# Kernel tuning notes

Measured on AMD Instinct MI355X. Metric: run time of the kernel, lower is better.

Reference implementation:

```python
import jax, jax.numpy as jnp
import numpy as np

B, D, FH, FW, C = 8, 41, 32, 88, 64
OGFH, OGFW = 512, 1408
DX = jnp.array([0.5, 20.0, 0.5], dtype=jnp.float32)          # voxel sizes (x, y, z)
BX = jnp.array([-49.75, 0.0, -49.75], dtype=jnp.float32)    # voxel centers origin
NX = (200, 1, 200)                                           # grid dims (x, y, z)
NSEG = NX[0] * NX[1] * NX[2] * B                             # 320000 voxel-batch slots


def _frustum():
    # (D, FH, FW, 3) pixel-u, pixel-v, depth; matches create_frustum_1camera
    ds = jnp.broadcast_to(jnp.arange(4.0, 45.0, 1.0)[:, None, None], (D, FH, FW))
    xs = jnp.broadcast_to(jnp.linspace(0.0, OGFW - 1, FW)[None, None, :], (D, FH, FW))
    ys = jnp.broadcast_to(jnp.linspace(0.0, OGFH - 1, FH)[None, :, None], (D, FH, FW))
    return jnp.stack([xs, ys, ds], axis=-1).astype(jnp.float32)


def setup_inputs() -> dict:
    key = jax.random.key(0)
    k1, = jax.random.split(key, 1)
    x = jax.random.normal(k1, (B, D, FH, FW, C), dtype=jnp.float32)
    # realistic pinhole intrinsics: fx=fy=800, principal point at image center
    K = np.array([[800.0, 0.0, OGFW / 2.0],
                  [0.0, 800.0, OGFH / 2.0],
                  [0.0, 0.0, 1.0]], dtype=np.float32)
    intrins = jnp.asarray(np.broadcast_to(K, (B, 3, 3)).copy())
    post_rots = jnp.broadcast_to(jnp.eye(3, dtype=jnp.float32), (B, 3, 3)) + jnp.zeros((B, 3, 3), jnp.float32)
    post_trans = jnp.zeros((B, 3), dtype=jnp.float32)
    return {"x": x, "intrins": intrins, "post_rots": post_rots, "post_trans": post_trans}


def _forward(x, intrins, post_rots, post_trans):
    # ---- get_geometry ----
    pts = _frustum()[None] - post_trans[:, None, None, None, :]          # (B,D,FH,FW,3)
    pts = jnp.einsum('bij,bdhwj->bdhwi', jnp.linalg.inv(post_rots), pts)
    pts = jnp.concatenate([pts[..., :2] * pts[..., 2:3], pts[..., 2:3]], axis=-1)
    geom = jnp.einsum('bij,bdhwj->bdhwi', jnp.linalg.inv(intrins), pts)  # camera-frame xyz

    # ---- voxel_splat ----
    Nprime = B * D * FH * FW
    xf = x.reshape(Nprime, C)
    # torch .long() truncates toward zero -> float->int cast in jnp also truncates
    coords = ((geom - (BX - DX / 2.0)) / DX).reshape(Nprime, 3).astype(jnp.int32)
    batch_ix = jnp.repeat(jnp.arange(B, dtype=jnp.int32), Nprime // B)
    kept = ((coords[:, 0] >= 0) & (coords[:, 0] < NX[0]) &
            (coords[:, 1] >= 0) & (coords[:, 1] < NX[1]) &
            (coords[:, 2] >= 0) & (coords[:, 2] < NX[2]))
    ranks = (coords[:, 0] * (NX[1] * NX[2] * B) + coords[:, 1] * (NX[2] * B) +
             coords[:, 2] * B + batch_ix)
    ranks = jnp.where(kept, ranks, NSEG)  # dump out-of-grid points into extra segment
    # segment-sum == sort + cumsum-trick pooling (sum of features per voxel)
    pooled = jax.ops.segment_sum(xf, ranks, num_segments=NSEG + 1)[:-1]  # (NSEG, C)
    final = pooled.reshape(NX[0], NX[1], NX[2], B, C)       # rank order: (x, y, z, b)
    final = jnp.transpose(final, (3, 4, 1, 2, 0))            # (B, C, ny, nz, nx)
    # torch.cat(final.unbind(dim=2), 1) -> stack ny slices along channel dim
    out = jnp.transpose(final, (0, 2, 1, 3, 4)).reshape(B, NX[1] * C, NX[2], NX[0])
    return out


def reference(x, intrins, post_rots, post_trans):
    return _forward(x, intrins, post_rots, post_trans)
```

## Files before the change

### kernel.cpp

```cpp
#include <hip/hip_runtime.h>

#define BB 8
#define DD 41
#define FHH 32
#define FWW 88
#define CC 64
#define NXX 200
#define NXZ 200
#define PLANE (NXZ * NXX)
#define WG 8
#define NWG (FWW / WG)
#define NBD (BB * DD)
#define NTILE (NBD * NWG)
#define NROWS (BB * NXZ)
#define PAD 204
#define STEPX (1407.0f / 87.0f)
#define STEPY (511.0f / 31.0f)

#define TSN    (NBD * FWW * CC)
#define MM_OFF TSN
#define CX_OFF (MM_OFF + NBD * FWW)
#define RD_OFF (CX_OFF + NBD * FWW)

__device__ __forceinline__ void inv3x3(const float* __restrict__ a, float* o) {
#pragma clang fp contract(off)
    float c00 = a[4] * a[8] - a[5] * a[7];
    float c01 = a[5] * a[6] - a[3] * a[8];
    float c02 = a[3] * a[7] - a[4] * a[6];
    float det = a[0] * c00 + a[1] * c01 + a[2] * c02;
    o[0] = c00 / det;
    o[1] = (a[2] * a[7] - a[1] * a[8]) / det;
    o[2] = (a[1] * a[5] - a[2] * a[4]) / det;
    o[3] = c01 / det;
    o[4] = (a[0] * a[8] - a[2] * a[6]) / det;
    o[5] = (a[2] * a[3] - a[0] * a[5]) / det;
    o[6] = c02 / det;
    o[7] = (a[1] * a[6] - a[0] * a[7]) / det;
    o[8] = (a[0] * a[4] - a[1] * a[3]) / det;
}

__device__ __forceinline__ int cz_of(const float* iR, const float* iK,
                                     float t0, float t1, float t2, int d) {
#pragma clang fp contract(off)
    float dv = 4.0f + (float)d;
    float q0 = 0.0f - t0, q1 = 0.0f - t1, q2 = dv - t2;
    float p0 = fmaf(iR[2], q2, fmaf(iR[1], q1, iR[0] * q0));
    float p1 = fmaf(iR[5], q2, fmaf(iR[4], q1, iR[3] * q0));
    float p2 = fmaf(iR[8], q2, fmaf(iR[7], q1, iR[6] * q0));
    float s0 = p0 * p2, s1 = p1 * p2, s2 = p2;
    float g2 = fmaf(iK[8], s2, fmaf(iK[7], s1, iK[6] * s0));
    float czf = (g2 + 50.0f) * 2.0f;
    return (int)czf;
}

__global__ __launch_bounds__(256) void lss_meta(
        const float* __restrict__ intrins, const float* __restrict__ post_rots,
        const float* __restrict__ post_trans, int* __restrict__ wsI) {
#pragma clang fp contract(off)
    __shared__ float sInv[18];
    int bd = blockIdx.x;
    int d = bd % DD, b = bd / DD;
    int tid = threadIdx.x;
    if (tid == 0) {
        inv3x3(post_rots + b * 9, sInv);
        inv3x3(intrins  + b * 9, sInv + 9);
    }
    __syncthreads();
    const float* iR = sInv;
    const float* iK = sInv + 9;
    float t0 = post_trans[b * 3 + 0];
    float t1 = post_trans[b * 3 + 1];
    float t2 = post_trans[b * 3 + 2];
    float dv = 4.0f + (float)d;
    unsigned* maskW = (unsigned*)wsI + MM_OFF;
    int* cxW  = wsI + CX_OFF;
    int* rowD = wsI + RD_OFF;

    for (int t = tid; t < FWW * FHH; t += 256) {
        int w = t >> 5;
        int h = t & 31;
        float u = (float)w * STEPX;
        float v = (float)h * STEPY;
        float q0 = u - t0, q1 = v - t1, q2 = dv - t2;
        float p0 = fmaf(iR[2], q2, fmaf(iR[1], q1, iR[0] * q0));
        float p1 = fmaf(iR[5], q2, fmaf(iR[4], q1, iR[3] * q0));
        float p2 = fmaf(iR[8], q2, fmaf(iR[7], q1, iR[6] * q0));
        float s0 = p0 * p2, s1 = p1 * p2, s2 = p2;
        float g0 = fmaf(iK[2], s2, fmaf(iK[1], s1, iK[0] * s0));
        float g1 = fmaf(iK[5], s2, fmaf(iK[4], s1, iK[3] * s0));
        float g2 = fmaf(iK[8], s2, fmaf(iK[7], s1, iK[6] * s0));
        float cxf = (g0 + 50.0f) * 2.0f;
        float cyf = (g1 + 10.0f) / 20.0f;
        float czf = (g2 + 50.0f) * 2.0f;
        int cx = (int)cxf;
        int cy = (int)cyf;
        int cz = (int)czf;
        bool kept = (cx >= 0) & (cx < NXX) & (cy == 0) & (cz >= 0) & (cz < NXZ);
        unsigned long long m = __ballot(kept);
        int lane = tid & 63;
        int cxc = min(NXX - 1, max(0, cx));
        if (lane == 0) {
            maskW[bd * FWW + w] = (unsigned)m;
            cxW[bd * FWW + w]   = cxc;
        } else if (lane == 32) {
            maskW[bd * FWW + w] = (unsigned)(m >> 32);
            cxW[bd * FWW + w]   = cxc;
        }
    }
    if (tid == 0) {
        int cz = cz_of(iR, iK, t0, t1, t2, d);
        if (cz >= 0 && cz < NXZ) rowD[b * NXZ + cz] = d;
    }
}

__global__ __launch_bounds__(512) void lss_tiles(
        const float* __restrict__ x, const int* __restrict__ wsI,
        float* __restrict__ wsF) {
#pragma clang fp contract(off)
    int blk = blockIdx.x;
    int tid = threadIdx.x;
    int wg = blk % NWG;
    int bd = blk / NWG;
    int wv   = tid >> 6;
    int lane = tid & 63;
    int cq   = lane & 15;
    int hsub = lane >> 4;
    int w = wg * WG + wv;

    unsigned m = ((const unsigned*)wsI)[MM_OFF + bd * FWW + w];
    const float* colp = x + ((size_t)bd * FHH * FWW + w) * CC + cq * 4;

    float4 vals[8];
#pragma unroll
    for (int hh = 0; hh < 8; ++hh)
        vals[hh] = *reinterpret_cast<const float4*>(
            colp + (size_t)(hh * 4 + hsub) * (FWW * CC));

    float4 acc = make_float4(0.f, 0.f, 0.f, 0.f);
#pragma unroll
    for (int hh = 0; hh < 8; ++hh) {
        bool bt = (m >> (hh * 4 + hsub)) & 1u;
        acc.x += bt ? vals[hh].x : 0.0f;
        acc.y += bt ? vals[hh].y : 0.0f;
        acc.z += bt ? vals[hh].z : 0.0f;
        acc.w += bt ? vals[hh].w : 0.0f;
    }
#pragma unroll
    for (int mm = 16; mm <= 32; mm <<= 1) {
        acc.x += __shfl_xor(acc.x, mm, 64);
        acc.y += __shfl_xor(acc.y, mm, 64);
        acc.z += __shfl_xor(acc.z, mm, 64);
        acc.w += __shfl_xor(acc.w, mm, 64);
    }
    if (hsub == 0)
        *reinterpret_cast<float4*>(wsF + ((size_t)(bd * FWW + w)) * CC + cq * 4) = acc;
}

__global__ __launch_bounds__(256) void lss_rows(
        const int* __restrict__ wsI, const float* __restrict__ wsF,
        float* __restrict__ out) {
#pragma clang fp contract(off)
    __shared__ float srow[CC * PAD];
    __shared__ int scx[FWW];
    int blk = blockIdx.x;
    int b = blk / NXZ, czr = blk % NXZ;
    int tid = threadIdx.x;
    int d = wsI[RD_OFF + blk];
    size_t outBase = ((size_t)b * CC) * PLANE + (size_t)czr * NXX;

    if (d < 0 || d >= DD) {
        float4 z = make_float4(0.f, 0.f, 0.f, 0.f);
        for (int i = tid; i < CC * (NXX / 4); i += 256) {
            int c = i / (NXX / 4), q = i - c * (NXX / 4);
            *reinterpret_cast<float4*>(out + outBase + (size_t)c * PLANE + q * 4) = z;
        }
        return;
    }
    int bd = b * DD + d;
    for (int i = tid; i < CC * PAD; i += 256) srow[i] = 0.0f;
    if (tid < FWW) scx[tid] = wsI[CX_OFF + bd * FWW + tid];
    __syncthreads();

    for (int i = tid; i < FWW * CC; i += 256) {
        int w = i >> 6, ch = i & 63;
        float v = wsF[(size_t)(bd * FWW + w) * CC + ch];
        atomicAdd(&srow[ch * PAD + scx[w]], v);
    }
    __syncthreads();

    for (int i = tid; i < CC * (NXX / 4); i += 256) {
        int c = i / (NXX / 4), q = i - c * (NXX / 4);
        *reinterpret_cast<float4*>(out + outBase + (size_t)c * PLANE + q * 4) =
            *reinterpret_cast<const float4*>(&srow[c * PAD + q * 4]);
    }
}

extern "C" void kernel_launch(void* const* d_in, const int* in_sizes, int n_in,
                              void* d_out, int out_size, void* d_ws, size_t ws_size,
                              hipStream_t stream) {
    const float* x          = (const float*)d_in[0];
    const float* intrins    = (const float*)d_in[1];
    const float* post_rots  = (const float*)d_in[2];
    const float* post_trans = (const float*)d_in[3];
    float* out = (float*)d_out;
    int*   wsI = (int*)d_ws;
    float* wsF = (float*)d_ws;

    lss_meta <<<NBD,   256, 0, stream>>>(intrins, post_rots, post_trans, wsI);
    lss_tiles<<<NTILE, 512, 0, stream>>>(x, wsI, wsF);
    lss_rows <<<NROWS, 256, 0, stream>>>(wsI, wsF, out);
}
```

Baseline: 88.41 us.

## Fuse column reduction and row scatter into one kernel split by cx halves

Merges the tile-reduction and row-writing kernels into one launch. Each (b,d) slice is handled by two blocks that cover the lower and upper cx range around a midpoint computed in the meta kernel. Each block reduces its columns and accumulates them with shared-memory atomics, then writes the output row directly. Extra blocks zero the rows that no depth covers, and they recompute that coverage themselves. This removes the intermediate workspace round-trip and one launch, but each slice now runs on at most two blocks, which lowers parallelism, and the output writes become scalar.

```diff
diff --git a/kernel.cpp b/kernel.cpp
--- a/kernel.cpp
+++ b/kernel.cpp
@@ -8,35 +8,38 @@
 #define NXX 200
 #define NXZ 200
 #define PLANE (NXZ * NXX)
-#define WG 8
-#define NWG (FWW / WG)
 #define NBD (BB * DD)
-#define NTILE (NBD * NWG)
+#define NHALF (2 * NBD)
 #define NROWS (BB * NXZ)
+#define NWG 11
 #define PAD 204
 #define STEPX (1407.0f / 87.0f)
 #define STEPY (511.0f / 31.0f)
 
-#define TSN    (NBD * FWW * CC)
-#define MM_OFF TSN
-#define CX_OFF (MM_OFF + NBD * FWW)
-#define RD_OFF (CX_OFF + NBD * FWW)
-
-__device__ __forceinline__ void inv3x3(const float* __restrict__ a, float* o) {
+#define MM_OFF 0
+#define CX_OFF (NBD * FWW)
+#define CZ_OFF (2 * NBD * FWW)
+#define CS_OFF (CZ_OFF + NBD)
+
+__device__ __forceinline__ float invEntry(const float* __restrict__ a, int e) {
 #pragma clang fp contract(off)
     float c00 = a[4] * a[8] - a[5] * a[7];
     float c01 = a[5] * a[6] - a[3] * a[8];
     float c02 = a[3] * a[7] - a[4] * a[6];
     float det = a[0] * c00 + a[1] * c01 + a[2] * c02;
-    o[0] = c00 / det;
-    o[1] = (a[2] * a[7] - a[1] * a[8]) / det;
-    o[2] = (a[1] * a[5] - a[2] * a[4]) / det;
-    o[3] = c01 / det;
-    o[4] = (a[0] * a[8] - a[2] * a[6]) / det;
-    o[5] = (a[2] * a[3] - a[0] * a[5]) / det;
-    o[6] = c02 / det;
-    o[7] = (a[1] * a[6] - a[0] * a[7]) / det;
-    o[8] = (a[0] * a[4] - a[1] * a[3]) / det;
+    float num;
+    switch (e) {
+        case 0: num = c00; break;
+        case 1: num = a[2] * a[7] - a[1] * a[8]; break;
+        case 2: num = a[1] * a[5] - a[2] * a[4]; break;
+        case 3: num = c01; break;
+        case 4: num = a[0] * a[8] - a[2] * a[6]; break;
+        case 5: num = a[2] * a[3] - a[0] * a[5]; break;
+        case 6: num = c02; break;
+        case 7: num = a[1] * a[6] - a[0] * a[7]; break;
+        default: num = a[0] * a[4] - a[1] * a[3]; break;
+    }
+    return num / det;
 }
 
 __device__ __forceinline__ int cz_of(const float* iR, const float* iK,
@@ -58,13 +61,17 @@
         const float* __restrict__ post_trans, int* __restrict__ wsI) {
 #pragma clang fp contract(off)
     __shared__ float sInv[18];
+    __shared__ unsigned smask[FWW];
+    __shared__ int scx[FWW];
+    __shared__ int smin, smax;
     int bd = blockIdx.x;
     int d = bd % DD, b = bd / DD;
     int tid = threadIdx.x;
-    if (tid == 0) {
-        inv3x3(post_rots + b * 9, sInv);
-        inv3x3(intrins  + b * 9, sInv + 9);
-    }
+    if (tid < 18) {
+        const float* a = (tid < 9 ? post_rots : intrins) + b * 9;
+        sInv[tid] = invEntry(a, tid % 9);
+    }
+    if (tid == 0) { smin = 1 << 30; smax = -1; }
     __syncthreads();
     const float* iR = sInv;
     const float* iK = sInv + 9;
@@ -72,9 +79,6 @@
     float t1 = post_trans[b * 3 + 1];
     float t2 = post_trans[b * 3 + 2];
     float dv = 4.0f + (float)d;
-    unsigned* maskW = (unsigned*)wsI + MM_OFF;
-    int* cxW  = wsI + CX_OFF;
-    int* rowD = wsI + RD_OFF;
 
     for (int t = tid; t < FWW * FHH; t += 256) {
         int w = t >> 5;
@@ -100,98 +104,129 @@
         int lane = tid & 63;
         int cxc = min(NXX - 1, max(0, cx));
         if (lane == 0) {
-            maskW[bd * FWW + w] = (unsigned)m;
-            cxW[bd * FWW + w]   = cxc;
+            smask[w] = (unsigned)m;          scx[w] = cxc;
+            ((unsigned*)wsI)[MM_OFF + bd * FWW + w] = (unsigned)m;
+            wsI[CX_OFF + bd * FWW + w] = cxc;
         } else if (lane == 32) {
-            maskW[bd * FWW + w] = (unsigned)(m >> 32);
-            cxW[bd * FWW + w]   = cxc;
-        }
-    }
+            smask[w] = (unsigned)(m >> 32);  scx[w] = cxc;
+            ((unsigned*)wsI)[MM_OFF + bd * FWW + w] = (unsigned)(m >> 32);
+            wsI[CX_OFF + bd * FWW + w] = cxc;
+        }
+    }
+    __syncthreads();
+    if (tid < FWW && smask[tid]) {
+        atomicMin(&smin, scx[tid]);
+        atomicMax(&smax, scx[tid]);
+    }
+    __syncthreads();
     if (tid == 0) {
-        int cz = cz_of(iR, iK, t0, t1, t2, d);
-        if (cz >= 0 && cz < NXZ) rowD[b * NXZ + cz] = d;
-    }
-}
-
-__global__ __launch_bounds__(512) void lss_tiles(
+        wsI[CZ_OFF + bd] = cz_of(iR, iK, t0, t1, t2, d);
+        wsI[CS_OFF + bd] = (smax < 0) ? 0 : ((smin + smax + 1) >> 1);
+    }
+}
+
+__global__ __launch_bounds__(512) void lss_main(
         const float* __restrict__ x, const int* __restrict__ wsI,
-        float* __restrict__ wsF) {
-#pragma clang fp contract(off)
+        const float* __restrict__ intrins, const float* __restrict__ post_rots,
+        const float* __restrict__ post_trans, float* __restrict__ out) {
+#pragma clang fp contract(off)
+    __shared__ float srow[CC * PAD];
+    __shared__ unsigned sm[FWW];
+    __shared__ int scx[FWW];
+    __shared__ int sflag;
     int blk = blockIdx.x;
     int tid = threadIdx.x;
-    int wg = blk % NWG;
-    int bd = blk / NWG;
-    int wv   = tid >> 6;
-    int lane = tid & 63;
-    int cq   = lane & 15;
-    int hsub = lane >> 4;
-    int w = wg * WG + wv;
-
-    unsigned m = ((const unsigned*)wsI)[MM_OFF + bd * FWW + w];
-    const float* colp = x + ((size_t)bd * FHH * FWW + w) * CC + cq * 4;
-
-    float4 vals[8];
+
+    if (blk >= NHALF) {
+        int r = blk - NHALF;
+        int b = r / NXZ, czr = r - b * NXZ;
+        float* sInv = srow;
+        if (tid < 18) {
+            const float* a = (tid < 9 ? post_rots : intrins) + b * 9;
+            sInv[tid] = invEntry(a, tid % 9);
+        }
+        __syncthreads();
+        if (tid < 64) {
+            bool cov = false;
+            if (tid < DD)
+                cov = (cz_of(sInv, sInv + 9, post_trans[b * 3], post_trans[b * 3 + 1],
+                             post_trans[b * 3 + 2], tid) == czr);
+            unsigned long long m = __ballot(cov);
+            if (tid == 0) sflag = (m != 0ull);
+        }
+        __syncthreads();
+        if (sflag) return;
+        float4 z = make_float4(0.f, 0.f, 0.f, 0.f);
+        size_t base = ((size_t)b * CC) * PLANE + (size_t)czr * NXX;
+        for (int i = tid; i < CC * (NXX / 4); i += 512) {
+            int c = i / (NXX / 4), q = i - c * (NXX / 4);
+            *reinterpret_cast<float4*>(out + base + (size_t)c * PLANE + q * 4) = z;
+        }
+        return;
+    }
+
+    int bd = blk >> 1;
+    int half = blk & 1;
+    int b = bd / DD;
+    int cz = wsI[CZ_OFF + bd];
+    if (cz < 0 || cz >= NXZ) return;
+    int cxs = wsI[CS_OFF + bd];
+    int lo = half ? cxs : 0;
+    int hi = half ? NXX : cxs;
+    if (lo >= hi) return;
+
+    if (tid < FWW) {
+        sm[tid]  = ((const unsigned*)wsI)[MM_OFF + bd * FWW + tid];
+        scx[tid] = wsI[CX_OFF + bd * FWW + tid];
+    }
+    for (int i = tid; i < CC * PAD; i += 512) srow[i] = 0.0f;
+    __syncthreads();
+
+    int wv = tid >> 6, lane = tid & 63;
+    int cq = lane & 15, hsub = lane >> 4;
+
+    for (int k = 0; k < NWG; ++k) {
+        int w = wv + (k << 3);
+        unsigned m = sm[w];
+        int cx = scx[w];
+        if (!m || cx < lo || cx >= hi) continue;
+        const float* colp = x + ((size_t)bd * FHH * FWW + w) * CC + (cq << 2);
+        float4 vals[8];
 #pragma unroll
-    for (int hh = 0; hh < 8; ++hh)
-        vals[hh] = *reinterpret_cast<const float4*>(
-            colp + (size_t)(hh * 4 + hsub) * (FWW * CC));
-
-    float4 acc = make_float4(0.f, 0.f, 0.f, 0.f);
+        for (int hh = 0; hh < 8; ++hh)
+            vals[hh] = *reinterpret_cast<const float4*>(
+                colp + (size_t)((hh << 2) + hsub) * (FWW * CC));
+        float4 acc = make_float4(0.f, 0.f, 0.f, 0.f);
 #pragma unroll
-    for (int hh = 0; hh < 8; ++hh) {
-        bool bt = (m >> (hh * 4 + hsub)) & 1u;
-        acc.x += bt ? vals[hh].x : 0.0f;
-        acc.y += bt ? vals[hh].y : 0.0f;
-        acc.z += bt ? vals[hh].z : 0.0f;
-        acc.w += bt ? vals[hh].w : 0.0f;
-    }
+        for (int hh = 0; hh < 8; ++hh) {
+            bool bt = (m >> ((hh << 2) + hsub)) & 1u;
+            acc.x += bt ? vals[hh].x : 0.0f;
+            acc.y += bt ? vals[hh].y : 0.0f;
+            acc.z += bt ? vals[hh].z : 0.0f;
+            acc.w += bt ? vals[hh].w : 0.0f;
+        }
 #pragma unroll
-    for (int mm = 16; mm <= 32; mm <<= 1) {
-        acc.x += __shfl_xor(acc.x, mm, 64);
-        acc.y += __shfl_xor(acc.y, mm, 64);
-        acc.z += __shfl_xor(acc.z, mm, 64);
-        acc.w += __shfl_xor(acc.w, mm, 64);
-    }
-    if (hsub == 0)
-        *reinterpret_cast<float4*>(wsF + ((size_t)(bd * FWW + w)) * CC + cq * 4) = acc;
-}
-
-__global__ __launch_bounds__(256) void lss_rows(
-        const int* __restrict__ wsI, const float* __restrict__ wsF,
-        float* __restrict__ out) {
-#pragma clang fp contract(off)
-    __shared__ float srow[CC * PAD];
-    __shared__ int scx[FWW];
-    int blk = blockIdx.x;
-    int b = blk / NXZ, czr = blk % NXZ;
-    int tid = threadIdx.x;
-    int d = wsI[RD_OFF + blk];
-    size_t outBase = ((size_t)b * CC) * PLANE + (size_t)czr * NXX;
-
-    if (d < 0 || d >= DD) {
-        float4 z = make_float4(0.f, 0.f, 0.f, 0.f);
-        for (int i = tid; i < CC * (NXX / 4); i += 256) {
-            int c = i / (NXX / 4), q = i - c * (NXX / 4);
-            *reinterpret_cast<float4*>(out + outBase + (size_t)c * PLANE + q * 4) = z;
-        }
-        return;
-    }
-    int bd = b * DD + d;
-    for (int i = tid; i < CC * PAD; i += 256) srow[i] = 0.0f;
-    if (tid < FWW) scx[tid] = wsI[CX_OFF + bd * FWW + tid];
-    __syncthreads();
-
-    for (int i = tid; i < FWW * CC; i += 256) {
-        int w = i >> 6, ch = i & 63;
-        float v = wsF[(size_t)(bd * FWW + w) * CC + ch];
-        atomicAdd(&srow[ch * PAD + scx[w]], v);
-    }
-    __syncthreads();
-
-    for (int i = tid; i < CC * (NXX / 4); i += 256) {
-        int c = i / (NXX / 4), q = i - c * (NXX / 4);
-        *reinterpret_cast<float4*>(out + outBase + (size_t)c * PLANE + q * 4) =
-            *reinterpret_cast<const float4*>(&srow[c * PAD + q * 4]);
+        for (int mm = 16; mm <= 32; mm <<= 1) {
+            acc.x += __shfl_xor(acc.x, mm, 64);
+            acc.y += __shfl_xor(acc.y, mm, 64);
+            acc.z += __shfl_xor(acc.z, mm, 64);
+            acc.w += __shfl_xor(acc.w, mm, 64);
+        }
+        if (hsub == 0) {
+            atomicAdd(&srow[(cq * 4 + 0) * PAD + cx], acc.x);
+            atomicAdd(&srow[(cq * 4 + 1) * PAD + cx], acc.y);
+            atomicAdd(&srow[(cq * 4 + 2) * PAD + cx], acc.z);
+            atomicAdd(&srow[(cq * 4 + 3) * PAD + cx], acc.w);
+        }
+    }
+    __syncthreads();
+
+    int n = hi - lo;
+    size_t base = ((size_t)b * CC) * PLANE + (size_t)cz * NXX;
+    for (int j = tid; j < CC * n; j += 512) {
+        int ch = j / n;
+        int cell = lo + (j - ch * n);
+        out[base + (size_t)ch * PLANE + cell] = srow[ch * PAD + cell];
     }
 }
 
@@ -204,9 +239,8 @@
     const float* post_trans = (const float*)d_in[3];
     float* out = (float*)d_out;
     int*   wsI = (int*)d_ws;
-    float* wsF = (float*)d_ws;
-
-    lss_meta <<<NBD,   256, 0, stream>>>(intrins, post_rots, post_trans, wsI);
-    lss_tiles<<<NTILE, 512, 0, stream>>>(x, wsI, wsF);
-    lss_rows <<<NROWS, 256, 0, stream>>>(wsI, wsF, out);
-}
+
+    lss_meta<<<NBD, 256, 0, stream>>>(intrins, post_rots, post_trans, wsI);
+    lss_main<<<NHALF + NROWS, 512, 0, stream>>>(x, wsI, intrins, post_rots,
+                                                post_trans, out);
+}
```

Measured after the change: 76.81 us. 1.15x faster.
